# Performance work log

Measured on AMD Instinct MI355X. Metric: run time of the kernel, lower is better.

## Reference

```python
import jax, jax.numpy as jnp
import numpy as np
import math

NN_K = 32          # num_neighbor = ceil(k/dilation) = 32
MAP_SIZE = 32
GROUP = 4


def _fibonacci_sphere(samples):
    # matches fibonacci_sphere(samples, randomize=False): rnd = 1.0
    pts = [[0.0, 0.0, 0.0]]
    offset = 2.0 / samples
    increment = math.pi * (3.0 - math.sqrt(5.0))
    for i in range(samples - 1):
        y = i * offset - 1 + offset / 2.0
        r = math.sqrt(1.0 - y * y)
        phi = ((i + 1.0) % samples) * increment
        pts.append([math.cos(phi) * r, y, math.sin(phi) * r])
    return np.asarray(pts, dtype=np.float32)


def setup_inputs() -> dict:
    B, N, C_in, C_out = 8, 2048, 64, 128
    key = jax.random.key(0)
    ks = jax.random.split(key, 6)
    x = jax.random.normal(ks[0], (B, 3, N), dtype=jnp.float32)
    feature = jax.random.normal(ks[1], (B, C_in, N), dtype=jnp.float32)
    neigh_indexs = jax.random.randint(ks[2], (B, N, NN_K), 0, N, dtype=jnp.int32)
    B_rff = jax.random.normal(ks[3], (7, MAP_SIZE), dtype=jnp.float32)  # frozen RFF proj
    kernels = jnp.asarray(_fibonacci_sphere(NN_K).T)                    # [3, NN_K], frozen
    mlp_w = jax.random.normal(ks[4], (C_in, 2 * MAP_SIZE), dtype=jnp.float32) * 0.05
    mlp_b = jnp.zeros((C_in,), dtype=jnp.float32)
    conv_w = jax.random.normal(ks[5], (C_out, 2 * C_in * NN_K), dtype=jnp.float32) * 0.02
    conv_b = jnp.zeros((C_out,), dtype=jnp.float32)
    return {"x": x, "feature": feature, "neigh_indexs": neigh_indexs,
            "B_rff": B_rff, "kernels": kernels,
            "mlp_w": mlp_w, "mlp_b": mlp_b, "conv_w": conv_w, "conv_b": conv_b}


def _topkmax(perm):
    # two normalization passes over axis=1 (rows), squaring in between, then hard threshold
    perm = perm / (jnp.sum(perm, axis=1, keepdims=True) + 1e-6)
    perm = perm * perm
    perm = perm / (jnp.sum(perm, axis=1, keepdims=True) + 1e-6)
    return jnp.where(perm > 0.1, perm, 0.0)


def _paiconv(x, feature, neigh_indexs, B_rff, kernels, mlp_w, mlp_b, conv_w, conv_b):
    bsz, C, N = feature.shape           # B, num_feat, num_pts
    nn_k = neigh_indexs.shape[-1]
    xp = jnp.transpose(x, (0, 2, 1))    # [B, N, 3]

    # neighbor gather of coordinates -> [B*N, nn, 3]
    x_neighs = jax.vmap(lambda p, i: p[i])(xp, neigh_indexs).reshape(bsz * N, nn_k, 3)
    x_rep = jnp.broadcast_to(x_neighs[:, :1, :], x_neighs.shape)
    x_rel = x_neighs - x_rep
    x_dis = jnp.linalg.norm(x_rel, axis=-1, keepdims=True)

    # random Fourier features + 1x1 conv (mlp)
    pos = (2.0 * math.pi) * jnp.concatenate([x_rep, x_rel, x_dis], axis=-1)  # [BN, nn, 7]
    xf = pos @ B_rff                                                          # [BN, nn, 32]
    xf = jnp.concatenate([jnp.sin(xf), jnp.cos(xf)], axis=-1)                 # [BN, nn, 64]
    xf = jnp.einsum('oc,bnc->bon', mlp_w, xf) + mlp_b[None, :, None]          # [BN, C, nn]

    # neighbor gather of features -> [BN, C, nn], concat with positional feats
    fp = jnp.transpose(feature, (0, 2, 1))                                    # [B, N, C]
    f_nb = jax.vmap(lambda p, i: p[i])(fp, neigh_indexs).reshape(bsz * N, nn_k, C)
    feats = jnp.concatenate([jnp.transpose(f_nb, (0, 2, 1)), xf], axis=1)     # [BN, 2C, nn]

    # permutation/attention matrix
    one_pad = jnp.zeros((nn_k, nn_k), dtype=x.dtype).at[0, 0].set(1.0)
    perm = x_rel @ kernels + one_pad                                          # [BN, nn, nn]
    perm = jnp.where(perm > 0, perm, 0.0)
    perm = _topkmax(perm)

    if C > 3:  # static channel shuffle with group=4
        feats = feats.reshape(bsz * N, GROUP, 2 * C // GROUP, nn_k)
        feats = jnp.transpose(feats, (0, 2, 1, 3)).reshape(bsz * N, 2 * C, nn_k)

    feats = feats @ perm                                                      # [BN, 2C, nn]
    feats = feats.reshape(bsz * N, 2 * C * nn_k)
    out = feats @ conv_w.T + conv_b                                           # [BN, out_c]
    return jnp.transpose(out.reshape(bsz, N, -1), (0, 2, 1))                  # [B, out_c, N]


def reference(x, feature, neigh_indexs, B_rff, kernels, mlp_w, mlp_b, conv_w, conv_b):
    return _paiconv(x, feature, neigh_indexs, B_rff, kernels, mlp_w, mlp_b, conv_w, conv_b)
```

## Files before the change

kernel.cpp:

```cpp
#include <hip/hip_runtime.h>
#include <hip/hip_bf16.h>

typedef unsigned short ushort_t;
typedef __attribute__((ext_vector_type(8))) short short8;
typedef __attribute__((ext_vector_type(4))) float floatx4;

#define TWO_PI 6.28318530717958647692f

__device__ __forceinline__ float bf2f(ushort_t u) {
  union { unsigned u; float f; } v; v.u = ((unsigned)u) << 16; return v.f;
}
__device__ __forceinline__ unsigned pk(float a, float b) {
  union { __hip_bfloat162 h2; unsigned u; } v;
  v.h2 = __float22bfloat162_rn(make_float2(a, b));
  return v.u;
}
__device__ __forceinline__ float ldin(const void* p, int idx, bool bf) {
  return bf ? bf2f(((const ushort_t*)p)[idx]) : ((const float*)p)[idx];
}
__device__ __forceinline__ bool detect_bf16(const void* xv) {
  const ushort_t* us = (const ushort_t*)xv;
  unsigned u = us[threadIdx.x & 63];
  int e = (u >> 7) & 0xFF;
  bool good = (e >= 110) && (e <= 133);
  unsigned long long m = __ballot(good);
  return __builtin_popcountll(m) >= 52;
}
__device__ __forceinline__ uint4 pack8f(const float* p) {
  float4 a = *(const float4*)p, b = *(const float4*)(p + 4);
  uint4 r;
  r.x = pk(a.x, a.y); r.y = pk(a.z, a.w);
  r.z = pk(b.x, b.y); r.w = pk(b.z, b.w);
  return r;
}

__global__ __launch_bounds__(256) void paiconv_prep(
    const void* __restrict__ xprobe, const void* __restrict__ feat,
    ushort_t* __restrict__ Ft, const void* __restrict__ W,
    ushort_t* __restrict__ Wc)
{
  const bool bfm = detect_bf16(xprobe);
  const int t = threadIdx.x;
  __shared__ ushort_t tile[64 * 72];

  if (blockIdx.x >= 256) {
    int i = ((blockIdx.x - 256) * 256 + t) << 3;
    int n = i >> 12, rem = i & 4095;
    int c = rem >> 5, j = rem & 31;
    int src = (n << 12) + (((c & 31) * 4 + (c >> 5)) << 5) + j;
    if (bfm) *(uint4*)(Wc + i) = *(const uint4*)((const ushort_t*)W + src);
    else     *(uint4*)(Wc + i) = pack8f((const float*)W + src);
    return;
  }

  const int bb = blockIdx.x >> 5;
  const int n0 = (blockIdx.x & 31) << 6;
  {
    const int c = t & 63, ng = t >> 6;
    size_t base = (((size_t)(bb * 64 + c)) << 11) + n0 + (ng << 4);
    ushort_t v[16];
    if (bfm) {
      const ushort_t* fp_ = (const ushort_t*)feat + base;
      uint4 a = *(const uint4*)fp_, b2 = *(const uint4*)(fp_ + 8);
      unsigned uu[8] = {a.x, a.y, a.z, a.w, b2.x, b2.y, b2.z, b2.w};
#pragma unroll
      for (int e = 0; e < 8; ++e) {
        v[2 * e] = (ushort_t)(uu[e] & 0xffff);
        v[2 * e + 1] = (ushort_t)(uu[e] >> 16);
      }
    } else {
      const float* fp_ = (const float*)feat + base;
#pragma unroll
      for (int k = 0; k < 16; k += 2) {
        unsigned u = pk(fp_[k], fp_[k + 1]);
        v[k] = (ushort_t)(u & 0xffff);
        v[k + 1] = (ushort_t)(u >> 16);
      }
    }
#pragma unroll
    for (int k = 0; k < 16; ++k) tile[(ng * 16 + k) * 72 + c] = v[k];
  }
  __syncthreads();
  {
    const int nn = t >> 2, qtr = t & 3;
    uint4 w0 = *(const uint4*)(tile + nn * 72 + qtr * 16);
    uint4 w1 = *(const uint4*)(tile + nn * 72 + qtr * 16 + 8);
    ushort_t* dst = Ft + (((size_t)(bb * 2048 + n0 + nn)) << 6) + (qtr << 4);
    *(uint4*)dst = w0;
    *(uint4*)(dst + 8) = w1;
  }
}

#define SFPT 5184
__global__ __launch_bounds__(256) void paiconv_phase1(
    const void* __restrict__ x,
    const ushort_t* __restrict__ Ft,
    const int*  __restrict__ nbr,
    const void* __restrict__ Brff,
    const void* __restrict__ kern,
    const void* __restrict__ mlpw,
    const void* __restrict__ mlpb,
    ushort_t*   __restrict__ Ag)
{
  const bool bfm = detect_bf16(x);
  const int t = threadIdx.x;
  const int p0 = blockIdx.x << 1;
  const int b  = p0 >> 11;
  const int w = t >> 6, lane = t & 63, lrow = lane & 15, quad = lane >> 4;

  __shared__ ushort_t sRt[64 * 72];
  __shared__ ushort_t sF[SFPT];
  __shared__ ushort_t sP[2 * 32 * 40];
  __shared__ float sRel[2][32][3];
  __shared__ float sDis[2][32];
  __shared__ float sRep[2][3];
  __shared__ float sBr[224];

  const int gpt = t >> 7, gj = (t >> 2) & 31, gch = t & 3;
  const int gidx = nbr[((p0 + gpt) << 5) + gj];
  const ushort_t* gfr = Ft + (((size_t)(b * 2048 + gidx)) << 6) + (gch << 4);
  uint4 g0 = ((const uint4*)gfr)[0];
  uint4 g1 = ((const uint4*)gfr)[1];

  const int pj = t & 31;
  const float kn0 = ldin(kern, pj, bfm);
  const float kn1 = ldin(kern, 32 + pj, bfm);
  const float kn2 = ldin(kern, 64 + pj, bfm);
  const int mc = (w << 4) + lrow;
  const float bv = ldin(mlpb, mc, bfm);

  short8 mb0, mb1;
  if (bfm) {
    const ushort_t* mp = (const ushort_t*)mlpw + mc * 64;
    mb0 = *(const short8*)(mp + (quad << 3));
    mb1 = *(const short8*)(mp + 32 + (quad << 3));
  } else {
    const float* mp = (const float*)mlpw + mc * 64;
    uint4 u0 = pack8f(mp + (quad << 3));
    uint4 u1 = pack8f(mp + 32 + (quad << 3));
    mb0 = *(short8*)&u0;
    mb1 = *(short8*)&u1;
  }

  if (t < 224) sBr[t] = ldin(Brff, t, bfm);
  if (t < 64) {
    int pt = t >> 5, i = t & 31;
    int p = p0 + pt;
    int idx  = nbr[(p << 5) + i];
    int idx0 = nbr[(p << 5)];
    int xo = b * 6144;
    float rx = ldin(x, xo + idx0, bfm);
    float ry = ldin(x, xo + 2048 + idx0, bfm);
    float rz = ldin(x, xo + 4096 + idx0, bfm);
    float cx = ldin(x, xo + idx, bfm);
    float cy = ldin(x, xo + 2048 + idx, bfm);
    float cz = ldin(x, xo + 4096 + idx, bfm);
    float dx = cx - rx, dy = cy - ry, dz = cz - rz;
    sRel[pt][i][0] = dx; sRel[pt][i][1] = dy; sRel[pt][i][2] = dz;
    sDis[pt][i] = sqrtf(dx * dx + dy * dy + dz * dz);
    if (i == 0) { sRep[pt][0] = rx; sRep[pt][1] = ry; sRep[pt][2] = rz; }
  }
  __syncthreads();

  {
    int jn = t >> 2, mh = (t & 3) << 3;
    int pt = jn >> 5, j = jn & 31;
    float pos[7];
    pos[0] = TWO_PI * sRep[pt][0]; pos[1] = TWO_PI * sRep[pt][1];
    pos[2] = TWO_PI * sRep[pt][2];
    pos[3] = TWO_PI * sRel[pt][j][0]; pos[4] = TWO_PI * sRel[pt][j][1];
    pos[5] = TWO_PI * sRel[pt][j][2];
    pos[6] = TWO_PI * sDis[pt][j];
    unsigned sw[4], cw[4];
#pragma unroll
    for (int mm = 0; mm < 8; mm += 2) {
      float a0 = 0.f, a1 = 0.f;
#pragma unroll
      for (int d = 0; d < 7; ++d) {
        a0 += pos[d] * sBr[d * 32 + mh + mm];
        a1 += pos[d] * sBr[d * 32 + mh + mm + 1];
      }
      sw[mm >> 1] = pk(__sinf(a0), __sinf(a1));
      cw[mm >> 1] = pk(__cosf(a0), __cosf(a1));
    }
    ushort_t* rb = sRt + jn * 72;
    *(uint4*)(rb + mh)      = make_uint4(sw[0], sw[1], sw[2], sw[3]);
    *(uint4*)(rb + 32 + mh) = make_uint4(cw[0], cw[1], cw[2], cw[3]);
  }
  if (t < 128) {
    int pt = t >> 6, h = (t >> 5) & 1;
    float col[16];
    float s1 = 0.f;
#pragma unroll
    for (int il = 0; il < 16; ++il) {
      int i = h * 16 + il;
      float v = sRel[pt][i][0] * kn0 + sRel[pt][i][1] * kn1 + sRel[pt][i][2] * kn2;
      if (i == 0 && pj == 0) v += 1.0f;
      v = fmaxf(v, 0.f);
      col[il] = v; s1 += v;
    }
    s1 += __shfl_xor(s1, 32, 64);
    float inv1 = 1.0f / (s1 + 1e-6f);
    float s2 = 0.f;
#pragma unroll
    for (int il = 0; il < 16; ++il) { float v = col[il] * inv1; v = v * v; col[il] = v; s2 += v; }
    s2 += __shfl_xor(s2, 32, 64);
    float inv2 = 1.0f / (s2 + 1e-6f);
    unsigned pw[8];
#pragma unroll
    for (int il = 0; il < 16; il += 2) {
      float v0 = col[il] * inv2;     v0 = (v0 > 0.1f) ? v0 : 0.f;
      float v1 = col[il + 1] * inv2; v1 = (v1 > 0.1f) ? v1 : 0.f;
      pw[il >> 1] = pk(v0, v1);
    }
    ushort_t* dst = sP + pt * 1280 + pj * 40 + h * 16;
    *(uint4*)dst       = make_uint4(pw[0], pw[1], pw[2], pw[3]);
    *(uint4*)(dst + 8) = make_uint4(pw[4], pw[5], pw[6], pw[7]);
  }
  __syncthreads();

  const int rbase = (64 + mc) * 40 + ((4 + w) << 3);

#pragma unroll
  for (int pt = 0; pt < 2; ++pt) {
    {
#pragma unroll
      for (int half = 0; half < 2; ++half) {
        int mt = pt * 2 + half;
        const ushort_t* rp = sRt + (mt * 16 + lrow) * 72 + (quad << 3);
        short8 a0 = *(const short8*)rp;
        short8 a1 = *(const short8*)(rp + 32);
        floatx4 acc = {0.f, 0.f, 0.f, 0.f};
        acc = __builtin_amdgcn_mfma_f32_16x16x32_bf16(a0, mb0, acc, 0, 0, 0);
        acc = __builtin_amdgcn_mfma_f32_16x16x32_bf16(a1, mb1, acc, 0, 0, 0);
        int j0 = (half << 4) + (quad << 2);
        *(uint2*)(sF + rbase + j0) =
            make_uint2(pk(acc[0] + bv, acc[1] + bv), pk(acc[2] + bv, acc[3] + bv));
      }
      if (gpt == pt) {
        ushort_t* fp_ = sF + gch * 648 + gj;
        unsigned uu[8] = {g0.x, g0.y, g0.z, g0.w, g1.x, g1.y, g1.z, g1.w};
#pragma unroll
        for (int u = 0; u < 8; ++u) {
          fp_[(2 * u) * 40]     = (ushort_t)(uu[u] & 0xffff);
          fp_[(2 * u + 1) * 40] = (ushort_t)(uu[u] >> 16);
        }
      }
    }
    __syncthreads();

    {
      const ushort_t* Pp = sP + pt * 1280;
      short8 a0 = *(const short8*)(Pp + lrow * 40 + (quad << 3));
      short8 a1 = *(const short8*)(Pp + (16 + lrow) * 40 + (quad << 3));
      size_t prow = ((size_t)(p0 + pt)) << 12;
#pragma unroll
      for (int nt = 0; nt < 2; ++nt) {
        int blk = w * 2 + nt;
        int cidx = (blk << 4) + lrow;
        short8 bfg = *(const short8*)(sF + cidx * 40 + (blk << 3) + (quad << 3));
        floatx4 z = {0.f, 0.f, 0.f, 0.f};
        floatx4 c0 = __builtin_amdgcn_mfma_f32_16x16x32_bf16(a0, bfg, z, 0, 0, 0);
        floatx4 c1 = __builtin_amdgcn_mfma_f32_16x16x32_bf16(a1, bfg, z, 0, 0, 0);
        ushort_t* ad = Ag + prow + cidx * 32 + (quad << 2);
        *(uint2*)ad        = make_uint2(pk(c0[0], c0[1]), pk(c0[2], c0[3]));
        *(uint2*)(ad + 16) = make_uint2(pk(c1[0], c1[1]), pk(c1[2], c1[3]));
      }
    }
    if (pt == 0) __syncthreads();
  }
}

__global__ __launch_bounds__(256) void paiconv_gemm(
    const ushort_t* __restrict__ A,
    const ushort_t* __restrict__ Wc,
    float* __restrict__ part)
{
  __shared__ ushort_t lA[2][64 * 72];
  __shared__ ushort_t lB[2][128 * 72];
  const int m0 = blockIdx.x << 6;
  const int K0 = blockIdx.y << 11;
  const int t = threadIdx.x;
  const int w = t >> 6, lane = t & 63;
  const int wm = w & 1, wn = w >> 1, lrow = lane & 15, quad = lane >> 4;

  const int ar = t >> 2, ac = (t & 3) << 4;
  const int wr = t >> 1, wc = (t & 1) << 5;
  const ushort_t* Ap = A + (size_t)(m0 + ar) * 4096 + K0 + ac;
  const ushort_t* Wp = Wc + (size_t)wr * 4096 + K0 + wc;

  uint4 ea0 = *(const uint4*)Ap,        ea1 = *(const uint4*)(Ap + 8);
  uint4 eb0 = *(const uint4*)Wp,        eb1 = *(const uint4*)(Wp + 8);
  uint4 eb2 = *(const uint4*)(Wp + 16), eb3 = *(const uint4*)(Wp + 24);
  uint4 oa0 = *(const uint4*)(Ap + 64),      oa1 = *(const uint4*)(Ap + 72);
  uint4 ob0 = *(const uint4*)(Wp + 64),      ob1 = *(const uint4*)(Wp + 72);
  uint4 ob2 = *(const uint4*)(Wp + 80),      ob3 = *(const uint4*)(Wp + 88);

  floatx4 acc[2][4];
#pragma unroll
  for (int i = 0; i < 2; ++i)
#pragma unroll
    for (int j = 0; j < 4; ++j) acc[i][j] = (floatx4){0.f, 0.f, 0.f, 0.f};

  for (int kb = 0; kb < 32; kb += 2) {
    {
      ushort_t* la = lA[0];
      ushort_t* lb = lB[0];
      *(uint4*)(la + ar * 72 + ac)      = ea0;
      *(uint4*)(la + ar * 72 + ac + 8)  = ea1;
      *(uint4*)(lb + wr * 72 + wc)      = eb0;
      *(uint4*)(lb + wr * 72 + wc + 8)  = eb1;
      *(uint4*)(lb + wr * 72 + wc + 16) = eb2;
      *(uint4*)(lb + wr * 72 + wc + 24) = eb3;
      __syncthreads();
      if (kb + 2 < 32) {
        int off = (kb + 2) << 6;
        ea0 = *(const uint4*)(Ap + off);      ea1 = *(const uint4*)(Ap + off + 8);
        eb0 = *(const uint4*)(Wp + off);      eb1 = *(const uint4*)(Wp + off + 8);
        eb2 = *(const uint4*)(Wp + off + 16); eb3 = *(const uint4*)(Wp + off + 24);
      }
#pragma unroll
      for (int kk = 0; kk < 2; ++kk) {
        short8 af0 = *(const short8*)(la + ((wm << 5) + lrow) * 72 + (kk << 5) + (quad << 3));
        short8 af1 = *(const short8*)(la + ((wm << 5) + 16 + lrow) * 72 + (kk << 5) + (quad << 3));
#pragma unroll
        for (int ni = 0; ni < 4; ++ni) {
          short8 bf = *(const short8*)(lb + ((wn << 6) + (ni << 4) + lrow) * 72 +
                                       (kk << 5) + (quad << 3));
          acc[0][ni] = __builtin_amdgcn_mfma_f32_16x16x32_bf16(af0, bf, acc[0][ni], 0, 0, 0);
          acc[1][ni] = __builtin_amdgcn_mfma_f32_16x16x32_bf16(af1, bf, acc[1][ni], 0, 0, 0);
        }
      }
    }
    {
      ushort_t* la = lA[1];
      ushort_t* lb = lB[1];
      *(uint4*)(la + ar * 72 + ac)      = oa0;
      *(uint4*)(la + ar * 72 + ac + 8)  = oa1;
      *(uint4*)(lb + wr * 72 + wc)      = ob0;
      *(uint4*)(lb + wr * 72 + wc + 8)  = ob1;
      *(uint4*)(lb + wr * 72 + wc + 16) = ob2;
      *(uint4*)(lb + wr * 72 + wc + 24) = ob3;
      __syncthreads();
      if (kb + 3 < 32) {
        int off = (kb + 3) << 6;
        oa0 = *(const uint4*)(Ap + off);      oa1 = *(const uint4*)(Ap + off + 8);
        ob0 = *(const uint4*)(Wp + off);      ob1 = *(const uint4*)(Wp + off + 8);
        ob2 = *(const uint4*)(Wp + off + 16); ob3 = *(const uint4*)(Wp + off + 24);
      }
#pragma unroll
      for (int kk = 0; kk < 2; ++kk) {
        short8 af0 = *(const short8*)(la + ((wm << 5) + lrow) * 72 + (kk << 5) + (quad << 3));
        short8 af1 = *(const short8*)(la + ((wm << 5) + 16 + lrow) * 72 + (kk << 5) + (quad << 3));
#pragma unroll
        for (int ni = 0; ni < 4; ++ni) {
          short8 bf = *(const short8*)(lb + ((wn << 6) + (ni << 4) + lrow) * 72 +
                                       (kk << 5) + (quad << 3));
          acc[0][ni] = __builtin_amdgcn_mfma_f32_16x16x32_bf16(af0, bf, acc[0][ni], 0, 0, 0);
          acc[1][ni] = __builtin_amdgcn_mfma_f32_16x16x32_bf16(af1, bf, acc[1][ni], 0, 0, 0);
        }
      }
    }
  }

  float* dst = part + ((size_t)blockIdx.y << 21);
#pragma unroll
  for (int mi = 0; mi < 2; ++mi)
#pragma unroll
    for (int ni = 0; ni < 4; ++ni)
#pragma unroll
      for (int r = 0; r < 4; ++r) {
        int m = m0 + (wm << 5) + (mi << 4) + (quad << 2) + r;
        int n = (wn << 6) + (ni << 4) + lrow;
        dst[(size_t)m * 128 + n] = acc[mi][ni][r];
      }
}

__global__ __launch_bounds__(256) void paiconv_reduce(
    const void* __restrict__ xprobe, const float* __restrict__ part,
    const void* __restrict__ bias, void* __restrict__ out)
{
  const bool bfm = detect_bf16(xprobe);
  __shared__ float buf[128 * 65];
  const int m0 = blockIdx.x << 6;
  const int b = m0 >> 11, n0 = m0 & 2047;
  const int t = threadIdx.x;

#pragma unroll
  for (int i = 0; i < 8; ++i) {
    int idx = (i * 256 + t) << 2;
    int mt = idx >> 7, c = idx & 127;
    size_t o = (size_t)(m0 + mt) * 128 + c;
    float4 v0 = *(const float4*)(part + o);
    float4 v1 = *(const float4*)(part + (1u << 21) + o);
    buf[(c + 0) * 65 + mt] = v0.x + v1.x + ldin(bias, c + 0, bfm);
    buf[(c + 1) * 65 + mt] = v0.y + v1.y + ldin(bias, c + 1, bfm);
    buf[(c + 2) * 65 + mt] = v0.z + v1.z + ldin(bias, c + 2, bfm);
    buf[(c + 3) * 65 + mt] = v0.w + v1.w + ldin(bias, c + 3, bfm);
  }
  __syncthreads();
#pragma unroll
  for (int i = 0; i < 8; ++i) {
    int idx = (i * 256 + t) << 2;
    int c = idx >> 6, nl = idx & 63;
    float v0 = buf[c * 65 + nl], v1 = buf[c * 65 + nl + 1];
    float v2 = buf[c * 65 + nl + 2], v3 = buf[c * 65 + nl + 3];
    size_t o = (size_t)b * 262144 + (size_t)c * 2048 + n0 + nl;
    if (bfm) *(uint2*)((ushort_t*)out + o) = make_uint2(pk(v0, v1), pk(v2, v3));
    else     *(float4*)((float*)out + o) = make_float4(v0, v1, v2, v3);
  }
}

extern "C" void kernel_launch(void* const* d_in, const int* in_sizes, int n_in,
                              void* d_out, int out_size, void* d_ws, size_t ws_size,
                              hipStream_t stream) {
  const void* x     = d_in[0];
  const void* feat  = d_in[1];
  const int*  nbr   = (const int*)d_in[2];
  const void* Brff  = d_in[3];
  const void* kern  = d_in[4];
  const void* mlpw  = d_in[5];
  const void* mlpb  = d_in[6];
  const void* convw = d_in[7];
  const void* convb = d_in[8];

  char* ws = (char*)d_ws;
  ushort_t* A   = (ushort_t*)ws;
  ushort_t* Wcv = (ushort_t*)(ws + (size_t)134217728);
  float*    prt = (float*)(ws + (size_t)135266304);
  ushort_t* Ft  = (ushort_t*)(ws + (size_t)152043520);

  paiconv_prep<<<512, 256, 0, stream>>>(x, feat, Ft, convw, Wcv);
  paiconv_phase1<<<8192, 256, 0, stream>>>(x, Ft, nbr, Brff, kern, mlpw, mlpb, A);
  paiconv_gemm<<<dim3(256, 2, 1), 256, 0, stream>>>(A, Wcv, prt);
  paiconv_reduce<<<256, 256, 0, stream>>>(x, prt, convb, d_out);
}
```

Before: 165.3 us.

## Remove split-K and fuse bias/transpose epilogue into GEMM kernel

```diff
diff --git a/kernel.cpp b/kernel.cpp
--- a/kernel.cpp
+++ b/kernel.cpp
@@ -272,63 +272,60 @@
 }
 
 __global__ __launch_bounds__(256) void paiconv_gemm(
+    const void* __restrict__ xprobe,
     const ushort_t* __restrict__ A,
     const ushort_t* __restrict__ Wc,
-    float* __restrict__ part)
+    const void* __restrict__ bias,
+    void* __restrict__ out)
 {
-  __shared__ ushort_t lA[2][64 * 72];
+  const bool bfm = detect_bf16(xprobe);
+  __shared__ ushort_t lA[2][32 * 72];
   __shared__ ushort_t lB[2][128 * 72];
-  const int m0 = blockIdx.x << 6;
-  const int K0 = blockIdx.y << 11;
+  const int m0 = blockIdx.x << 5;
   const int t = threadIdx.x;
   const int w = t >> 6, lane = t & 63;
   const int wm = w & 1, wn = w >> 1, lrow = lane & 15, quad = lane >> 4;
 
-  const int ar = t >> 2, ac = (t & 3) << 4;
+  const int ar = t >> 3, ac = (t & 7) << 3;
   const int wr = t >> 1, wc = (t & 1) << 5;
-  const ushort_t* Ap = A + (size_t)(m0 + ar) * 4096 + K0 + ac;
-  const ushort_t* Wp = Wc + (size_t)wr * 4096 + K0 + wc;
-
-  uint4 ea0 = *(const uint4*)Ap,        ea1 = *(const uint4*)(Ap + 8);
+  const ushort_t* Ap = A + (size_t)(m0 + ar) * 4096 + ac;
+  const ushort_t* Wp = Wc + (size_t)wr * 4096 + wc;
+
+  uint4 ea0 = *(const uint4*)Ap;
   uint4 eb0 = *(const uint4*)Wp,        eb1 = *(const uint4*)(Wp + 8);
   uint4 eb2 = *(const uint4*)(Wp + 16), eb3 = *(const uint4*)(Wp + 24);
-  uint4 oa0 = *(const uint4*)(Ap + 64),      oa1 = *(const uint4*)(Ap + 72);
-  uint4 ob0 = *(const uint4*)(Wp + 64),      ob1 = *(const uint4*)(Wp + 72);
-  uint4 ob2 = *(const uint4*)(Wp + 80),      ob3 = *(const uint4*)(Wp + 88);
-
-  floatx4 acc[2][4];
-#pragma unroll
-  for (int i = 0; i < 2; ++i)
-#pragma unroll
-    for (int j = 0; j < 4; ++j) acc[i][j] = (floatx4){0.f, 0.f, 0.f, 0.f};
-
-  for (int kb = 0; kb < 32; kb += 2) {
+  uint4 oa0 = *(const uint4*)(Ap + 64);
+  uint4 ob0 = *(const uint4*)(Wp + 64), ob1 = *(const uint4*)(Wp + 72);
+  uint4 ob2 = *(const uint4*)(Wp + 80), ob3 = *(const uint4*)(Wp + 88);
+
+  floatx4 acc[4];
+#pragma unroll
+  for (int j = 0; j < 4; ++j) acc[j] = (floatx4){0.f, 0.f, 0.f, 0.f};
+
+  for (int kb = 0; kb < 64; kb += 2) {
     {
       ushort_t* la = lA[0];
       ushort_t* lb = lB[0];
       *(uint4*)(la + ar * 72 + ac)      = ea0;
-      *(uint4*)(la + ar * 72 + ac + 8)  = ea1;
       *(uint4*)(lb + wr * 72 + wc)      = eb0;
       *(uint4*)(lb + wr * 72 + wc + 8)  = eb1;
       *(uint4*)(lb + wr * 72 + wc + 16) = eb2;
       *(uint4*)(lb + wr * 72 + wc + 24) = eb3;
       __syncthreads();
-      if (kb + 2 < 32) {
+      if (kb + 2 < 64) {
         int off = (kb + 2) << 6;
-        ea0 = *(const uint4*)(Ap + off);      ea1 = *(const uint4*)(Ap + off + 8);
+        ea0 = *(const uint4*)(Ap + off);
         eb0 = *(const uint4*)(Wp + off);      eb1 = *(const uint4*)(Wp + off + 8);
         eb2 = *(const uint4*)(Wp + off + 16); eb3 = *(const uint4*)(Wp + off + 24);
       }
 #pragma unroll
       for (int kk = 0; kk < 2; ++kk) {
-        short8 af0 = *(const short8*)(la + ((wm << 5) + lrow) * 72 + (kk << 5) + (quad << 3));
-        short8 af1 = *(const short8*)(la + ((wm << 5) + 16 + lrow) * 72 + (kk << 5) + (quad << 3));
+        short8 af = *(const short8*)(la + ((wm << 4) + lrow) * 72 + (kk << 5) + (quad << 3));
 #pragma unroll
         for (int ni = 0; ni < 4; ++ni) {
           short8 bf = *(const short8*)(lb + ((wn << 6) + (ni << 4) + lrow) * 72 +
                                        (kk << 5) + (quad << 3));
-          acc[0][ni] = __builtin_amdgcn_mfma_f32_16x16x32_bf16(af0, bf, acc[0][ni], 0, 0, 0);
-          acc[1][ni] = __builtin_amdgcn_mfma_f32_16x16x32_bf16(af1, bf, acc[1][ni], 0, 0, 0);
+          acc[ni] = __builtin_amdgcn_mfma_f32_16x16x32_bf16(af, bf, acc[ni], 0, 0, 0);
         }
       }
     }
@@ -336,78 +333,41 @@
       ushort_t* la = lA[1];
       ushort_t* lb = lB[1];
       *(uint4*)(la + ar * 72 + ac)      = oa0;
-      *(uint4*)(la + ar * 72 + ac + 8)  = oa1;
       *(uint4*)(lb + wr * 72 + wc)      = ob0;
       *(uint4*)(lb + wr * 72 + wc + 8)  = ob1;
       *(uint4*)(lb + wr * 72 + wc + 16) = ob2;
       *(uint4*)(lb + wr * 72 + wc + 24) = ob3;
       __syncthreads();
-      if (kb + 3 < 32) {
+      if (kb + 3 < 64) {
         int off = (kb + 3) << 6;
-        oa0 = *(const uint4*)(Ap + off);      oa1 = *(const uint4*)(Ap + off + 8);
+        oa0 = *(const uint4*)(Ap + off);
         ob0 = *(const uint4*)(Wp + off);      ob1 = *(const uint4*)(Wp + off + 8);
         ob2 = *(const uint4*)(Wp + off + 16); ob3 = *(const uint4*)(Wp + off + 24);
       }
 #pragma unroll
       for (int kk = 0; kk < 2; ++kk) {
-        short8 af0 = *(const short8*)(la + ((wm << 5) + lrow) * 72 + (kk << 5) + (quad << 3));
-        short8 af1 = *(const short8*)(la + ((wm << 5) + 16 + lrow) * 72 + (kk << 5) + (quad << 3));
+        short8 af = *(const short8*)(la + ((wm << 4) + lrow) * 72 + (kk << 5) + (quad << 3));
 #pragma unroll
         for (int ni = 0; ni < 4; ++ni) {
           short8 bf = *(const short8*)(lb + ((wn << 6) + (ni << 4) + lrow) * 72 +
                                        (kk << 5) + (quad << 3));
-          acc[0][ni] = __builtin_amdgcn_mfma_f32_16x16x32_bf16(af0, bf, acc[0][ni], 0, 0, 0);
-          acc[1][ni] = __builtin_amdgcn_mfma_f32_16x16x32_bf16(af1, bf, acc[1][ni], 0, 0, 0);
+          acc[ni] = __builtin_amdgcn_mfma_f32_16x16x32_bf16(af, bf, acc[ni], 0, 0, 0);
         }
       }
     }
   }
 
-  float* dst = part + ((size_t)blockIdx.y << 21);
-#pragma unroll
-  for (int mi = 0; mi < 2; ++mi)
-#pragma unroll
-    for (int ni = 0; ni < 4; ++ni)
-#pragma unroll
-      for (int r = 0; r < 4; ++r) {
-        int m = m0 + (wm << 5) + (mi << 4) + (quad << 2) + r;
-        int n = (wn << 6) + (ni << 4) + lrow;
-        dst[(size_t)m * 128 + n] = acc[mi][ni][r];
-      }
-}
-
-__global__ __launch_bounds__(256) void paiconv_reduce(
-    const void* __restrict__ xprobe, const float* __restrict__ part,
-    const void* __restrict__ bias, void* __restrict__ out)
-{
-  const bool bfm = detect_bf16(xprobe);
-  __shared__ float buf[128 * 65];
-  const int m0 = blockIdx.x << 6;
   const int b = m0 >> 11, n0 = m0 & 2047;
-  const int t = threadIdx.x;
-
-#pragma unroll
-  for (int i = 0; i < 8; ++i) {
-    int idx = (i * 256 + t) << 2;
-    int mt = idx >> 7, c = idx & 127;
-    size_t o = (size_t)(m0 + mt) * 128 + c;
-    float4 v0 = *(const float4*)(part + o);
-    float4 v1 = *(const float4*)(part + (1u << 21) + o);
-    buf[(c + 0) * 65 + mt] = v0.x + v1.x + ldin(bias, c + 0, bfm);
-    buf[(c + 1) * 65 + mt] = v0.y + v1.y + ldin(bias, c + 1, bfm);
-    buf[(c + 2) * 65 + mt] = v0.z + v1.z + ldin(bias, c + 2, bfm);
-    buf[(c + 3) * 65 + mt] = v0.w + v1.w + ldin(bias, c + 3, bfm);
-  }
-  __syncthreads();
-#pragma unroll
-  for (int i = 0; i < 8; ++i) {
-    int idx = (i * 256 + t) << 2;
-    int c = idx >> 6, nl = idx & 63;
-    float v0 = buf[c * 65 + nl], v1 = buf[c * 65 + nl + 1];
-    float v2 = buf[c * 65 + nl + 2], v3 = buf[c * 65 + nl + 3];
-    size_t o = (size_t)b * 262144 + (size_t)c * 2048 + n0 + nl;
+  const int pr = (wm << 4) + (quad << 2);
+#pragma unroll
+  for (int ni = 0; ni < 4; ++ni) {
+    int ch = (wn << 6) + (ni << 4) + lrow;
+    float vb = ldin(bias, ch, bfm);
+    float v0 = acc[ni][0] + vb, v1 = acc[ni][1] + vb;
+    float v2 = acc[ni][2] + vb, v3 = acc[ni][3] + vb;
+    size_t o = (size_t)b * 262144 + (size_t)ch * 2048 + n0 + pr;
     if (bfm) *(uint2*)((ushort_t*)out + o) = make_uint2(pk(v0, v1), pk(v2, v3));
-    else     *(float4*)((float*)out + o) = make_float4(v0, v1, v2, v3);
+    else     *(float4*)((float*)out + o)   = make_float4(v0, v1, v2, v3);
   }
 }
 
@@ -427,11 +387,9 @@
   char* ws = (char*)d_ws;
   ushort_t* A   = (ushort_t*)ws;
   ushort_t* Wcv = (ushort_t*)(ws + (size_t)134217728);
-  float*    prt = (float*)(ws + (size_t)135266304);
   ushort_t* Ft  = (ushort_t*)(ws + (size_t)152043520);
 
   paiconv_prep<<<512, 256, 0, stream>>>(x, feat, Ft, convw, Wcv);
   paiconv_phase1<<<8192, 256, 0, stream>>>(x, Ft, nbr, Brff, kern, mlpw, mlpb, A);
-  paiconv_gemm<<<dim3(256, 2, 1), 256, 0, stream>>>(A, Wcv, prt);
-  paiconv_reduce<<<256, 256, 0, stream>>>(x, prt, convb, d_out);
-}
+  paiconv_gemm<<<512, 256, 0, stream>>>(x, A, Wcv, convb, d_out);
+}
```

After: 172.0 us. 4.0% more time.
